# Kernel optimization log

Measured on AMD Instinct MI355X. Metric: run time of the kernel, lower is better.

Reference implementation:

```python
import jax, jax.numpy as jnp
import numpy as np

N, R, T = 40000, 2000, 500000   # node_size, rel_size, triple_size
D, DEPTH, PROXY_N = 128, 2, 64  # node_F, depth, proxy rows
DC = D * (DEPTH + 1)            # 384


def _unique_edges(rng, n_rows, n_cols, n_edges):
    # sorted, duplicate-free edge list -> matches torch.sparse coalesce() ordering
    keys = np.unique(rng.integers(0, n_rows * n_cols, size=int(n_edges * 1.05), dtype=np.int64))[:n_edges]
    assert keys.shape[0] == n_edges
    return np.stack([keys // n_cols, keys % n_cols], axis=1)


def _init_emb(key, r, c):
    w = jax.random.normal(key, (r, c), dtype=jnp.float32)
    return w / jnp.maximum(jnp.linalg.norm(w, axis=1, keepdims=True), 1e-12)


def setup_inputs() -> dict:
    rng = np.random.default_rng(0)
    adj = jnp.asarray(_unique_edges(rng, N, N, T))                    # [T,2] (src, dst)
    idx = jnp.stack([jnp.arange(T), jnp.asarray(rng.integers(0, R, T, dtype=np.int64))], axis=1)  # [T,2]
    val = jnp.ones((T,), jnp.float32)
    ent_m = jnp.asarray(_unique_edges(rng, N, N, T))
    rel_m = jnp.asarray(_unique_edges(rng, N, R, T))
    ks = jax.random.split(jax.random.key(0), 12)
    return {
        "ent_emb": _init_emb(ks[0], N, D),
        "rel_emb": _init_emb(ks[1], R, D),
        "e_gate": _init_emb(ks[2], DC, DC),
        "e_proxy": _init_emb(ks[3], PROXY_N, DC),
        "e_bias": _init_emb(ks[4], 1, DC),
        "e_attn": jnp.stack([_init_emb(ks[5], D, 1), _init_emb(ks[6], D, 1)]),
        "r_gate": _init_emb(ks[7], DC, DC),
        "r_proxy": _init_emb(ks[8], PROXY_N, DC),
        "r_bias": _init_emb(ks[9], 1, DC),
        "r_attn": jnp.stack([_init_emb(ks[10], D, 1), _init_emb(ks[11], D, 1)]),
        "val_input": val,
        "adj_input": adj,
        "index_input": idx,
        "ent_matrix": ent_m,
        "rel_matrix": rel_m,
    }


def _l2(x):
    return x / jnp.maximum(jnp.linalg.norm(x, axis=-1, keepdims=True), 1e-12)


def _seg_softmax(v, seg, n):
    m = jax.ops.segment_max(v, seg, num_segments=n)
    e = jnp.exp(v - m[seg])
    s = jax.ops.segment_sum(e, seg, num_segments=n)
    return e / s[seg]


def _adj_agg(edges, emb, n_rows):
    # torch.sparse.softmax over rows of an all-ones adjacency, then sparse @ emb
    rows, cols = edges[:, 0], edges[:, 1]
    w = _seg_softmax(jnp.zeros(edges.shape[0], emb.dtype), rows, n_rows)
    return jax.ops.segment_sum(w[:, None] * emb[cols], rows, num_segments=n_rows)


def _graph_attention(features, rel_emb, edges, sp_idx, sp_val, attn, gate_k, proxy, bias):
    n = features.shape[0]
    t = sp_val.shape[0]
    feats = jnp.tanh(features)
    outs = [feats]
    for l in range(DEPTH):
        # sparse (T,R) @ rel_emb -> per-edge relation embedding, then L2 normalize
        rels_sum = _l2(jax.ops.segment_sum(sp_val[:, None] * rel_emb[sp_idx[:, 1]], sp_idx[:, 0], num_segments=t))
        neighs = feats[edges[:, 1]]                                   # [T,D]
        neighs = neighs - 2.0 * jnp.sum(neighs * rels_sum, axis=1, keepdims=True) * rels_sum  # Householder reflection
        att = _seg_softmax((rels_sum @ attn[l])[:, 0], edges[:, 0], n)  # sparse row softmax
        feats = jnp.tanh(jax.ops.segment_sum(neighs * att[:, None], edges[:, 0], num_segments=n))
        outs.append(feats)
    outputs = jnp.concatenate(outs, axis=1)                           # [N, DC]
    pa = jax.nn.softmax(_l2(outputs) @ _l2(proxy).T, axis=-1)         # [N, 64]
    pf = outputs - pa @ proxy
    gate = jax.nn.sigmoid(pf @ gate_k + bias)
    return gate * outputs + (1.0 - gate) * pf


def reference(ent_emb, rel_emb, e_gate, e_proxy, e_bias, e_attn, r_gate, r_proxy, r_bias, r_attn, val_input, adj_input, index_input, ent_matrix, rel_matrix):
    ent_feature = _adj_agg(ent_matrix, ent_emb, N)                    # [N,D]
    rel_feature = _adj_agg(rel_matrix, rel_emb, N)                    # [N,D]
    out_e = _graph_attention(ent_feature, rel_emb, adj_input, index_input, val_input, e_attn, e_gate, e_proxy, e_bias)
    out_r = _graph_attention(rel_feature, rel_emb, adj_input, index_input, val_input, r_attn, r_gate, r_proxy, r_bias)
    # dropout_rate = 0.0 -> identity
    return jnp.concatenate([out_e, out_r], axis=-1)                   # [N, 2*DC]
```

## Files before the change

### kernel.cpp

```cpp
#include <hip/hip_runtime.h>
#include <hip/hip_fp16.h>


typedef __attribute__((ext_vector_type(4))) float f32x4;
typedef _Float16 h16x2 __attribute__((ext_vector_type(2)));
typedef _Float16 f16x8 __attribute__((ext_vector_type(8)));
typedef float f32x16 __attribute__((ext_vector_type(16)));

__device__ __forceinline__ float wave_sum(float v) {
#pragma unroll
  for (int o = 32; o > 0; o >>= 1) v += __shfl_xor(v, o, 64);
  return v;
}
__device__ __forceinline__ float wave_max(float v) {
#pragma unroll
  for (int o = 32; o > 0; o >>= 1) v = fmaxf(v, __shfl_xor(v, o, 64));
  return v;
}
__device__ __forceinline__ unsigned pkhalf2(float a, float b) {
  __half2 h = __floats2half2_rn(a, b);
  return __builtin_bit_cast(unsigned, h);
}
__device__ __forceinline__ float bcf(unsigned u) {
  return __builtin_bit_cast(float, u);
}
__device__ __forceinline__ unsigned short f2h(float x) {
  return __builtin_bit_cast(unsigned short, (_Float16)x);
}
__device__ __forceinline__ float h2f(unsigned short h) {
  return (float)__builtin_bit_cast(_Float16, h);
}
__device__ __forceinline__ float tanh_fast(float x) {
  float t = __expf(-2.f * fabsf(x));
  float y = (1.f - t) / (1.f + t);
  return copysignf(y, x);
}
__device__ __forceinline__ float fdot2u(unsigned a, unsigned b, float c) {
#if __has_builtin(__builtin_amdgcn_fdot2)
  return __builtin_amdgcn_fdot2(__builtin_bit_cast(h16x2, a),
                                __builtin_bit_cast(h16x2, b), c, false);
#else
  h16x2 x = __builtin_bit_cast(h16x2, a), y = __builtin_bit_cast(h16x2, b);
  return fmaf((float)x.x, (float)y.x, fmaf((float)x.y, (float)y.y, c));
#endif
}

__global__ void rowptr3_kernel(const int* __restrict__ e0,
                               const int* __restrict__ e1,
                               const int* __restrict__ e2, int T, int N,
                               int* __restrict__ p0, int* __restrict__ p1,
                               int* __restrict__ p2) {
  int tid = blockIdx.x * blockDim.x + threadIdx.x;
  int which = tid / (N + 1);
  int r = tid - which * (N + 1);
  if (which >= 3) return;
  const int* E = which == 0 ? e0 : (which == 1 ? e1 : e2);
  int* P = which == 0 ? p0 : (which == 1 ? p1 : p2);
  int lo = 0, hi = T;
  while (lo < hi) {
    int mid = (lo + hi) >> 1;
    if (E[2 * mid] < r) lo = mid + 1; else hi = mid;
  }
  P[r] = lo;
}

__global__ void relprep_kernel(const float* __restrict__ rel_emb,
                               const float* __restrict__ e_attn,
                               const float* __restrict__ r_attn, int R,
                               float* __restrict__ srel,
                               unsigned* __restrict__ rnorm,
                               unsigned* __restrict__ rel16) {
  int r = blockIdx.x * 4 + (threadIdx.x >> 6);
  int lane = threadIdx.x & 63;
  if (r >= R) return;
  float2 v  = *(const float2*)(rel_emb + (size_t)r * 128 + 2 * lane);
  float2 a0 = *(const float2*)(e_attn + 2 * lane);
  float2 a1 = *(const float2*)(e_attn + 128 + 2 * lane);
  float2 b0 = *(const float2*)(r_attn + 2 * lane);
  float2 b1 = *(const float2*)(r_attn + 128 + 2 * lane);
  float n  = wave_sum(v.x * v.x + v.y * v.y);
  float d0 = wave_sum(v.x * a0.x + v.y * a0.y);
  float d1 = wave_sum(v.x * a1.x + v.y * a1.y);
  float d2 = wave_sum(v.x * b0.x + v.y * b0.y);
  float d3 = wave_sum(v.x * b1.x + v.y * b1.y);
  float inv = 1.f / fmaxf(sqrtf(n), 1e-12f);
  rnorm[(size_t)r * 64 + lane] = pkhalf2(v.x * inv, v.y * inv);
  rel16[(size_t)r * 64 + lane] = pkhalf2(v.x, v.y);
  if (lane == 0) {
    srel[r]          = d0 * inv;
    srel[R + r]      = d1 * inv;
    srel[2 * R + r]  = d2 * inv;
    srel[3 * R + r]  = d3 * inv;
  }
}

__global__ void pack_f16_kernel(const float* __restrict__ src,
                                unsigned* __restrict__ dst, int n2) {
  int i = blockIdx.x * blockDim.x + threadIdx.x;
  if (i >= n2) return;
  float2 v = *(const float2*)(src + 2 * (size_t)i);
  dst[i] = pkhalf2(v.x, v.y);
}

__global__ __launch_bounds__(256) void stats_kernel(
    const int* __restrict__ ptr, const int* __restrict__ idx,
    const float* __restrict__ srel, int R, float* __restrict__ stats, int N) {
  int r = blockIdx.x * 4 + (threadIdx.x >> 6);
  if (r >= N) return;
  int lane = threadIdx.x & 63;
  int beg = ptr[r], end = ptr[r + 1];
  const float* s0 = srel;
  const float* s1 = srel + R;
  const float* s2 = srel + 2 * R;
  const float* s3 = srel + 3 * R;
  float m0 = -INFINITY, m1 = -INFINITY, m2 = -INFINITY, m3 = -INFINITY;
  for (int e = beg + lane; e < end; e += 64) {
    int rel = idx[2 * e + 1];
    m0 = fmaxf(m0, s0[rel]); m1 = fmaxf(m1, s1[rel]);
    m2 = fmaxf(m2, s2[rel]); m3 = fmaxf(m3, s3[rel]);
  }
#pragma unroll
  for (int o = 32; o > 0; o >>= 1) {
    m0 = fmaxf(m0, __shfl_xor(m0, o, 64));
    m1 = fmaxf(m1, __shfl_xor(m1, o, 64));
    m2 = fmaxf(m2, __shfl_xor(m2, o, 64));
    m3 = fmaxf(m3, __shfl_xor(m3, o, 64));
  }
  float d0 = 0.f, d1 = 0.f, d2 = 0.f, d3 = 0.f;
  for (int e = beg + lane; e < end; e += 64) {
    int rel = idx[2 * e + 1];
    d0 += __expf(s0[rel] - m0); d1 += __expf(s1[rel] - m1);
    d2 += __expf(s2[rel] - m2); d3 += __expf(s3[rel] - m3);
  }
#pragma unroll
  for (int o = 32; o > 0; o >>= 1) {
    d0 += __shfl_xor(d0, o, 64); d1 += __shfl_xor(d1, o, 64);
    d2 += __shfl_xor(d2, o, 64); d3 += __shfl_xor(d3, o, 64);
  }
  if (lane == 0) {
    float4 a, b;
    a.x = m0; a.y = (d0 > 0.f) ? 1.f / d0 : 0.f;
    a.z = m1; a.w = (d1 > 0.f) ? 1.f / d1 : 0.f;
    b.x = m2; b.y = (d2 > 0.f) ? 1.f / d2 : 0.f;
    b.z = m3; b.w = (d3 > 0.f) ? 1.f / d3 : 0.f;
    *(float4*)(stats + (size_t)r * 8) = a;
    *(float4*)(stats + (size_t)r * 8 + 4) = b;
  }
}

__global__ void weight_kernel(const int* __restrict__ adj,
                              const int* __restrict__ idx,
                              const float* __restrict__ srel, int R,
                              const float* __restrict__ stats,
                              unsigned* __restrict__ pk,
                              uint2* __restrict__ wt0,
                              uint2* __restrict__ wt1, int T) {
  int e = blockIdx.x * blockDim.x + threadIdx.x;
  if (e >= T) return;
  int row = adj[2 * e];
  int col = adj[2 * e + 1];
  int rel = idx[2 * e + 1];
  float4 a = *(const float4*)(stats + (size_t)row * 8);
  float4 b = *(const float4*)(stats + (size_t)row * 8 + 4);
  float w0 = __expf(srel[rel] - a.x) * a.y;
  float w1 = __expf(srel[R + rel] - a.z) * a.w;
  float w2 = __expf(srel[2 * R + rel] - b.x) * b.y;
  float w3 = __expf(srel[3 * R + rel] - b.z) * b.w;
  pk[e] = (unsigned)col | ((unsigned)rel << 16);
  wt0[e] = make_uint2(__builtin_bit_cast(unsigned, w0),
                      __builtin_bit_cast(unsigned, w2));
  wt1[e] = make_uint2(__builtin_bit_cast(unsigned, w1),
                      __builtin_bit_cast(unsigned, w3));
}

__global__ __launch_bounds__(256) void agg_fused_kernel(
    const int* __restrict__ ptrE, const int* __restrict__ edgesE,
    const unsigned* __restrict__ ent16, const int* __restrict__ ptrR,
    const int* __restrict__ edgesR, const unsigned* __restrict__ rel16,
    unsigned* __restrict__ fout, int N) {
  int r = blockIdx.x * 4 + (threadIdx.x >> 6);
  if (r >= N) return;
  int lane = threadIdx.x & 63;
  int g = lane >> 4, q = lane & 15;

  float aE[8] = {0, 0, 0, 0, 0, 0, 0, 0};
  float aR[8] = {0, 0, 0, 0, 0, 0, 0, 0};

  auto addh = [&](uint4 u, float* a) {
    h16x2 h0 = __builtin_bit_cast(h16x2, u.x), h1 = __builtin_bit_cast(h16x2, u.y);
    h16x2 h2 = __builtin_bit_cast(h16x2, u.z), h3 = __builtin_bit_cast(h16x2, u.w);
    a[0] += (float)h0.x; a[1] += (float)h0.y;
    a[2] += (float)h1.x; a[3] += (float)h1.y;
    a[4] += (float)h2.x; a[5] += (float)h2.y;
    a[6] += (float)h3.x; a[7] += (float)h3.y;
  };

  int begE = ptrE[r], endE = ptrE[r + 1];
  for (int e0 = begE; e0 < endE; e0 += 8) {
    int eA = e0 + g, eB = e0 + 4 + g;
    if (eA < endE)
      addh(*(const uint4*)(ent16 + (size_t)edgesE[2 * eA + 1] * 64 + 4 * q), aE);
    if (eB < endE)
      addh(*(const uint4*)(ent16 + (size_t)edgesE[2 * eB + 1] * 64 + 4 * q), aE);
  }
  int begR = ptrR[r], endR = ptrR[r + 1];
  for (int e0 = begR; e0 < endR; e0 += 8) {
    int eA = e0 + g, eB = e0 + 4 + g;
    if (eA < endR)
      addh(*(const uint4*)(rel16 + (size_t)edgesR[2 * eA + 1] * 64 + 4 * q), aR);
    if (eB < endR)
      addh(*(const uint4*)(rel16 + (size_t)edgesR[2 * eB + 1] * 64 + 4 * q), aR);
  }
#pragma unroll
  for (int j = 0; j < 8; ++j) {
    aE[j] += __shfl_xor(aE[j], 16, 64); aE[j] += __shfl_xor(aE[j], 32, 64);
    aR[j] += __shfl_xor(aR[j], 16, 64); aR[j] += __shfl_xor(aR[j], 32, 64);
  }
  float sE = (endE > begE) ? 1.f / (float)(endE - begE) : 0.f;
  float sR = (endR > begR) ? 1.f / (float)(endR - begR) : 0.f;
  if (g == 0) {
    float t[8];
#pragma unroll
    for (int j = 0; j < 8; ++j) t[j] = tanh_fast(aE[j] * sE);
    uint4 u;
    u.x = pkhalf2(t[0], t[1]); u.y = pkhalf2(t[2], t[3]);
    u.z = pkhalf2(t[4], t[5]); u.w = pkhalf2(t[6], t[7]);
    *(uint4*)(fout + (size_t)r * 128 + 4 * q) = u;
  } else if (g == 1) {
    float t[8];
#pragma unroll
    for (int j = 0; j < 8; ++j) t[j] = tanh_fast(aR[j] * sR);
    uint4 u;
    u.x = pkhalf2(t[0], t[1]); u.y = pkhalf2(t[2], t[3]);
    u.z = pkhalf2(t[4], t[5]); u.w = pkhalf2(t[6], t[7]);
    *(uint4*)(fout + (size_t)r * 128 + 64 + 4 * q) = u;
  }
}

__global__ __launch_bounds__(256) void layer_rec_kernel(
    const int* __restrict__ ptr, const unsigned* __restrict__ pk,
    const uint2* __restrict__ wt, const unsigned* __restrict__ rnorm,
    const unsigned* __restrict__ fin, unsigned* __restrict__ fout,
    int fstride, int N) {
  int r = blockIdx.x * 4 + (threadIdx.x >> 6);
  if (r >= N) return;
  int lane = threadIdx.x & 63;
  int g = lane >> 4, q = lane & 15;
  int beg = ptr[r], end = ptr[r + 1];

  float aE[8] = {0, 0, 0, 0, 0, 0, 0, 0};
  float aR[8] = {0, 0, 0, 0, 0, 0, 0, 0};

  auto accum = [&](uint4 F, uint4 V, float w, float s, float* a) {
    h16x2 f0 = __builtin_bit_cast(h16x2, F.x), v0 = __builtin_bit_cast(h16x2, V.x);
    h16x2 f1 = __builtin_bit_cast(h16x2, F.y), v1 = __builtin_bit_cast(h16x2, V.y);
    h16x2 f2 = __builtin_bit_cast(h16x2, F.z), v2 = __builtin_bit_cast(h16x2, V.z);
    h16x2 f3 = __builtin_bit_cast(h16x2, F.w), v3 = __builtin_bit_cast(h16x2, V.w);
    a[0] = fmaf((float)f0.x, w, fmaf((float)v0.x, s, a[0]));
    a[1] = fmaf((float)f0.y, w, fmaf((float)v0.y, s, a[1]));
    a[2] = fmaf((float)f1.x, w, fmaf((float)v1.x, s, a[2]));
    a[3] = fmaf((float)f1.y, w, fmaf((float)v1.y, s, a[3]));
    a[4] = fmaf((float)f2.x, w, fmaf((float)v2.x, s, a[4]));
    a[5] = fmaf((float)f2.y, w, fmaf((float)v2.y, s, a[5]));
    a[6] = fmaf((float)f3.x, w, fmaf((float)v3.x, s, a[6]));
    a[7] = fmaf((float)f3.y, w, fmaf((float)v3.y, s, a[7]));
  };

  for (int e0 = beg; e0 < end; e0 += 8) {
    int eA = e0 + g, eB = e0 + 4 + g;
    bool actA = eA < end, actB = eB < end;
    unsigned pkA = actA ? pk[eA] : 0u;
    unsigned pkB = actB ? pk[eB] : 0u;
    uint2 wA = actA ? wt[eA] : make_uint2(0u, 0u);
    uint2 wB = actB ? wt[eB] : make_uint2(0u, 0u);
    int colA = (int)(pkA & 0xFFFFu), relA = (int)(pkA >> 16);
    int colB = (int)(pkB & 0xFFFFu), relB = (int)(pkB >> 16);
    float wAE = bcf(wA.x), wAR = bcf(wA.y);
    float wBE = bcf(wB.x), wBR = bcf(wB.y);

    const unsigned* fA = fin + (size_t)colA * 128;
    const unsigned* fB = fin + (size_t)colB * 128;
    uint4 EA = *(const uint4*)(fA + 4 * q);
    uint4 RA = *(const uint4*)(fA + 64 + 4 * q);
    uint4 VA = *(const uint4*)(rnorm + (size_t)relA * 64 + 4 * q);
    uint4 EB = *(const uint4*)(fB + 4 * q);
    uint4 RB = *(const uint4*)(fB + 64 + 4 * q);
    uint4 VB = *(const uint4*)(rnorm + (size_t)relB * 64 + 4 * q);

    float dAE = fdot2u(EA.w, VA.w, fdot2u(EA.z, VA.z,
                fdot2u(EA.y, VA.y, fdot2u(EA.x, VA.x, 0.f))));
    float dAR = fdot2u(RA.w, VA.w, fdot2u(RA.z, VA.z,
                fdot2u(RA.y, VA.y, fdot2u(RA.x, VA.x, 0.f))));
    float dBE = fdot2u(EB.w, VB.w, fdot2u(EB.z, VB.z,
                fdot2u(EB.y, VB.y, fdot2u(EB.x, VB.x, 0.f))));
    float dBR = fdot2u(RB.w, VB.w, fdot2u(RB.z, VB.z,
                fdot2u(RB.y, VB.y, fdot2u(RB.x, VB.x, 0.f))));
#pragma unroll
    for (int m = 1; m < 16; m <<= 1) {
      dAE += __shfl_xor(dAE, m, 64);
      dAR += __shfl_xor(dAR, m, 64);
      dBE += __shfl_xor(dBE, m, 64);
      dBR += __shfl_xor(dBR, m, 64);
    }
    float sAE = -2.f * wAE * dAE, sAR = -2.f * wAR * dAR;
    float sBE = -2.f * wBE * dBE, sBR = -2.f * wBR * dBR;
    accum(EA, VA, wAE, sAE, aE);
    accum(RA, VA, wAR, sAR, aR);
    accum(EB, VB, wBE, sBE, aE);
    accum(RB, VB, wBR, sBR, aR);
  }

#pragma unroll
  for (int j = 0; j < 8; ++j) {
    aE[j] += __shfl_xor(aE[j], 16, 64); aE[j] += __shfl_xor(aE[j], 32, 64);
    aR[j] += __shfl_xor(aR[j], 16, 64); aR[j] += __shfl_xor(aR[j], 32, 64);
  }
  if (g == 0) {
    float t[8];
#pragma unroll
    for (int j = 0; j < 8; ++j) t[j] = tanh_fast(aE[j]);
    uint4 u;
    u.x = pkhalf2(t[0], t[1]); u.y = pkhalf2(t[2], t[3]);
    u.z = pkhalf2(t[4], t[5]); u.w = pkhalf2(t[6], t[7]);
    *(uint4*)(fout + (size_t)r * fstride + 4 * q) = u;
  } else if (g == 1) {
    float t[8];
#pragma unroll
    for (int j = 0; j < 8; ++j) t[j] = tanh_fast(aR[j]);
    uint4 u;
    u.x = pkhalf2(t[0], t[1]); u.y = pkhalf2(t[2], t[3]);
    u.z = pkhalf2(t[4], t[5]); u.w = pkhalf2(t[6], t[7]);
    *(uint4*)(fout + (size_t)r * fstride + 64 + 4 * q) = u;
  }
}

__device__ __forceinline__ void pack_one32(const float* __restrict__ src,
                                           unsigned short* __restrict__ dst,
                                           int NT, int srcld, int mode, int f,
                                           int lane) {
  int kt = f / NT, nt = f % NT;
  int kbase = 16 * kt + 8 * (lane >> 5);
  int n = 32 * nt + (lane & 31);
  unsigned short tmp[8];
#pragma unroll
  for (int j = 0; j < 8; ++j) {
    int k = kbase + j;
    float v = (mode == 0) ? src[(size_t)k * srcld + n] : src[(size_t)n * srcld + k];
    tmp[j] = f2h(v);
  }
  *(uint4*)(dst + ((size_t)f * 64 + lane) * 8) = *(uint4*)tmp;
}
__global__ void pack_all_kernel(const float* eP, const float* eG,
                                const float* rP, const float* rG,
                                unsigned short* b1e, unsigned short* b2e,
                                unsigned short* b3e, unsigned short* b1r,
                                unsigned short* b2r, unsigned short* b3r) {
  int f = blockIdx.x * 4 + (threadIdx.x >> 6);
  int lane = threadIdx.x & 63;
  if (f < 48)       pack_one32(eP, b1e, 2, 384, 1, f, lane);
  else if (f < 96)  pack_one32(eP, b2e, 12, 384, 0, f - 48, lane);
  else if (f < 384) pack_one32(eG, b3e, 12, 384, 0, f - 96, lane);
  else if (f < 432) pack_one32(rP, b1r, 2, 384, 1, f - 384, lane);
  else if (f < 480) pack_one32(rP, b2r, 12, 384, 0, f - 432, lane);
  else if (f < 768) pack_one32(rG, b3r, 12, 384, 0, f - 480, lane);
}

__global__ __launch_bounds__(512) void final_v4_kernel(
    const unsigned* __restrict__ f0, const unsigned* __restrict__ f1,
    const unsigned* __restrict__ f2, int s2, int plane,
    const unsigned short* __restrict__ B1, const unsigned short* __restrict__ B2,
    const unsigned short* __restrict__ B3, const float* __restrict__ bias,
    float* __restrict__ gout, int coloff) {
  __shared__ __align__(16) unsigned sOutH[64][204];
  __shared__ __align__(16) float sPa[64][68];
  __shared__ __align__(16) unsigned short sPaH[64][72];
  __shared__ float sInv[64];
  unsigned short* sOutHs = (unsigned short*)&sOutH[0][0];

  const int t = threadIdx.x;
  const int w = t >> 6, lane = t & 63;
  const int l31 = lane & 31, l5 = lane >> 5;
  const int row0 = blockIdx.x * 64;

  for (int i = t; i < 64 * 48; i += 512) {
    int r = i / 48, c4 = i % 48;
    int buf = c4 >> 4, j = c4 & 15;
    const unsigned* src;
    if (buf == 0)      src = f0 + (size_t)(row0 + r) * 128 + plane + 4 * j;
    else if (buf == 1) src = f1 + (size_t)(row0 + r) * 128 + plane + 4 * j;
    else               src = f2 + (size_t)(row0 + r) * s2 + plane + 4 * j;
    *(uint4*)&sOutH[r][c4 * 4] = *(const uint4*)src;
  }
  __syncthreads();

  for (int rr = 8 * w; rr < 8 * w + 8; ++rr) {
    float s = 0.f;
#pragma unroll
    for (int k = 0; k < 3; ++k) {
      unsigned u = sOutH[rr][3 * lane + k];
      s = fdot2u(u, u, s);
    }
    s = wave_sum(s);
    if (lane == 0) sInv[rr] = 1.f / fmaxf(sqrtf(s), 1e-12f);
  }
  __syncthreads();

  if (w < 4) {
    int rt = w >> 1, ct = w & 1;
    f32x16 acc = {0.f, 0.f, 0.f, 0.f, 0.f, 0.f, 0.f, 0.f,
                  0.f, 0.f, 0.f, 0.f, 0.f, 0.f, 0.f, 0.f};
#pragma unroll
    for (int kt = 0; kt < 24; ++kt) {
      f16x8 a = __builtin_bit_cast(
          f16x8, *(const uint4*)&sOutH[rt * 32 + l31][8 * kt + 4 * l5]);
      f16x8 b = *(const f16x8*)(B1 + ((size_t)(kt * 2 + ct) * 64 + lane) * 8);
      acc = __builtin_amdgcn_mfma_f32_32x32x16_f16(a, b, acc, 0, 0, 0);
    }
#pragma unroll
    for (int reg = 0; reg < 16; ++reg) {
      int row = rt * 32 + (reg & 3) + 8 * (reg >> 2) + 4 * l5;
      sPa[row][ct * 32 + l31] = acc[reg] * sInv[row];
    }
  }
  __syncthreads();

  for (int rr = 8 * w; rr < 8 * w + 8; ++rr) {
    float v = sPa[rr][lane];
    float mx = wave_max(v);
    float e = __expf(v - mx);
    float s = wave_sum(e);
    sPaH[rr][lane] = f2h(e / s);
  }
  __syncthreads();

  const int rt = w & 1, ntb = 3 * (w >> 1);
  unsigned outv[3][8];
  {
    f32x16 acc2[3];
#pragma unroll
    for (int s = 0; s < 3; ++s)
#pragma unroll
      for (int i = 0; i < 16; ++i) acc2[s][i] = 0.f;
#pragma unroll
    for (int kt = 0; kt < 4; ++kt) {
      f16x8 a = __builtin_bit_cast(
          f16x8, *(const uint4*)&sPaH[rt * 32 + l31][16 * kt + 8 * l5]);
#pragma unroll
      for (int s = 0; s < 3; ++s) {
        f16x8 b = *(const f16x8*)(B2 + ((size_t)(kt * 12 + ntb + s) * 64 + lane) * 8);
        acc2[s] = __builtin_amdgcn_mfma_f32_32x32x16_f16(a, b, acc2[s], 0, 0, 0);
      }
    }
#pragma unroll
    for (int s = 0; s < 3; ++s) {
      int col = 32 * (ntb + s) + l31;
#pragma unroll
      for (int p = 0; p < 8; ++p) {
        int ra = rt * 32 + ((2 * p) & 3) + 8 * (p >> 1) + 4 * l5;
        unsigned short u0 = sOutHs[ra * 408 + col];
        unsigned short u1 = sOutHs[(ra + 1) * 408 + col];
        outv[s][p] = (unsigned)u0 | ((unsigned)u1 << 16);
        float pf0 = h2f(u0) - acc2[s][2 * p];
        float pf1 = h2f(u1) - acc2[s][2 * p + 1];
        sOutHs[ra * 408 + col] = f2h(pf0);
        sOutHs[(ra + 1) * 408 + col] = f2h(pf1);
      }
    }
  }
  __syncthreads();

  f32x16 acc3[3];
#pragma unroll
  for (int s = 0; s < 3; ++s)
#pragma unroll
    for (int i = 0; i < 16; ++i) acc3[s][i] = 0.f;
#pragma unroll
  for (int kt = 0; kt < 24; ++kt) {
    f16x8 a = __builtin_bit_cast(
        f16x8, *(const uint4*)&sOutH[rt * 32 + l31][8 * kt + 4 * l5]);
#pragma unroll
    for (int s = 0; s < 3; ++s) {
      f16x8 b = *(const f16x8*)(B3 + ((size_t)(kt * 12 + ntb + s) * 64 + lane) * 8);
      acc3[s] = __builtin_amdgcn_mfma_f32_32x32x16_f16(a, b, acc3[s], 0, 0, 0);
    }
  }

#pragma unroll
  for (int s = 0; s < 3; ++s) {
    int col = 32 * (ntb + s) + l31;
    float bv = bias[col];
#pragma unroll
    for (int p = 0; p < 8; ++p) {
      int ra = rt * 32 + ((2 * p) & 3) + 8 * (p >> 1) + 4 * l5;
      float g0 = 1.f / (1.f + __expf(-(acc3[s][2 * p] + bv)));
      float g1 = 1.f / (1.f + __expf(-(acc3[s][2 * p + 1] + bv)));
      float pf0 = h2f(sOutHs[ra * 408 + col]);
      float pf1 = h2f(sOutHs[(ra + 1) * 408 + col]);
      unsigned ov = outv[s][p];
      float o0 = h2f((unsigned short)(ov & 0xffffu));
      float o1 = h2f((unsigned short)(ov >> 16));
      gout[(size_t)(row0 + ra) * 768 + coloff + col] = g0 * o0 + (1.f - g0) * pf0;
      gout[(size_t)(row0 + ra + 1) * 768 + coloff + col] =
          g1 * o1 + (1.f - g1) * pf1;
    }
  }
}

extern "C" void kernel_launch(void* const* d_in, const int* in_sizes, int n_in,
                              void* d_out, int out_size, void* d_ws,
                              size_t ws_size, hipStream_t stream) {
  (void)n_in; (void)out_size; (void)ws_size;
  const float* ent_emb = (const float*)d_in[0];
  const float* rel_emb = (const float*)d_in[1];
  const float* e_gate  = (const float*)d_in[2];
  const float* e_proxy = (const float*)d_in[3];
  const float* e_bias  = (const float*)d_in[4];
  const float* e_attn  = (const float*)d_in[5];
  const float* r_gate  = (const float*)d_in[6];
  const float* r_proxy = (const float*)d_in[7];
  const float* r_bias  = (const float*)d_in[8];
  const float* r_attn  = (const float*)d_in[9];
  const int* adj   = (const int*)d_in[11];
  const int* idx   = (const int*)d_in[12];
  const int* ent_m = (const int*)d_in[13];
  const int* rel_m = (const int*)d_in[14];
  const int N = in_sizes[0] / 128;
  const int R = in_sizes[1] / 128;
  const int T = in_sizes[10];
  float* out = (float*)d_out;

  char* w = (char*)d_ws;
  size_t used = 0;
  auto alloc = [&](size_t bytes) {
    void* p = (void*)(w + used);
    used += (bytes + 255) & ~(size_t)255;
    return p;
  };
  int* ptr_adj  = (int*)alloc((size_t)(N + 1) * sizeof(int));
  int* ptr_ent  = (int*)alloc((size_t)(N + 1) * sizeof(int));
  int* ptr_rel  = (int*)alloc((size_t)(N + 1) * sizeof(int));
  float* srel   = (float*)alloc((size_t)4 * R * sizeof(float));
  unsigned short* b1e = (unsigned short*)alloc(48 * 1024);
  unsigned short* b2e = (unsigned short*)alloc(48 * 1024);
  unsigned short* b3e = (unsigned short*)alloc(288 * 1024);
  unsigned short* b1r = (unsigned short*)alloc(48 * 1024);
  unsigned short* b2r = (unsigned short*)alloc(48 * 1024);
  unsigned short* b3r = (unsigned short*)alloc(288 * 1024);
  unsigned* rnorm = (unsigned*)alloc((size_t)R * 64 * 4);
  unsigned* rel16 = (unsigned*)alloc((size_t)R * 64 * 4);
  unsigned* ent16 = (unsigned*)alloc((size_t)N * 64 * 4);
  unsigned* fsrc0 = (unsigned*)alloc((size_t)N * 128 * 4);
  unsigned* fsrc1 = (unsigned*)alloc((size_t)N * 128 * 4);
  float* stats = (float*)alloc((size_t)N * 8 * sizeof(float));
  unsigned* pk = (unsigned*)alloc((size_t)T * 4);
  uint2* wt0 = (uint2*)alloc((size_t)T * 8);
  uint2* wt1 = (uint2*)alloc((size_t)T * 8);

  dim3 b256(256);
  rowptr3_kernel<<<(3 * (N + 1) + 255) / 256, b256, 0, stream>>>(
      adj, ent_m, rel_m, T, N, ptr_adj, ptr_ent, ptr_rel);
  relprep_kernel<<<(R + 3) / 4, b256, 0, stream>>>(rel_emb, e_attn, r_attn, R,
                                                   srel, rnorm, rel16);
  pack_f16_kernel<<<(N * 64 + 255) / 256, b256, 0, stream>>>(ent_emb, ent16,
                                                             N * 64);
  pack_all_kernel<<<192, b256, 0, stream>>>(e_proxy, e_gate, r_proxy, r_gate,
                                            b1e, b2e, b3e, b1r, b2r, b3r);

  int grow = (N + 3) / 4;
  stats_kernel<<<grow, b256, 0, stream>>>(ptr_adj, idx, srel, R, stats, N);
  weight_kernel<<<(T + 255) / 256, b256, 0, stream>>>(adj, idx, srel, R, stats,
                                                      pk, wt0, wt1, T);
  agg_fused_kernel<<<grow, b256, 0, stream>>>(ptr_ent, ent_m, ent16, ptr_rel,
                                              rel_m, rel16, fsrc0, N);
  unsigned* gscratch = (unsigned*)out + 512;
  layer_rec_kernel<<<grow, b256, 0, stream>>>(ptr_adj, pk, wt0, rnorm, fsrc0,
                                              fsrc1, 128, N);
  layer_rec_kernel<<<grow, b256, 0, stream>>>(ptr_adj, pk, wt1, rnorm, fsrc1,
                                              gscratch, 768, N);

  int fblocks = (N + 63) / 64;
  final_v4_kernel<<<fblocks, dim3(512), 0, stream>>>(
      fsrc0, fsrc1, gscratch, 768, 0, b1e, b2e, b3e, e_bias, out, 0);
  final_v4_kernel<<<fblocks, dim3(512), 0, stream>>>(
      fsrc0, fsrc1, gscratch, 768, 64, b1r, b2r, b3r, r_bias, out, 384);
}
```

Baseline: 351.6 us.

## Merge entity and relation final kernels into one launch with 32-row blocks

The two final_v4 launches become one final_fused_kernel. Each 256-thread block handles 32 rows for either the entity or the relation side, and the block index picks which. The row L2 norm is now computed while the tile is loaded into shared memory, which removes a separate pass and a barrier. The layer-2 scratch moves to out columns 0 and 704 so each side's writes never overwrite scratch the other side still needs to read. This cuts one kernel launch and the tail between the two launches, and smaller blocks raise occupancy, at the cost of reloading the B matrices per smaller tile.

```diff
diff --git a/kernel.cpp b/kernel.cpp
--- a/kernel.cpp
+++ b/kernel.cpp
@@ -240,8 +240,8 @@
 __global__ __launch_bounds__(256) void layer_rec_kernel(
     const int* __restrict__ ptr, const unsigned* __restrict__ pk,
     const uint2* __restrict__ wt, const unsigned* __restrict__ rnorm,
-    const unsigned* __restrict__ fin, unsigned* __restrict__ fout,
-    int fstride, int N) {
+    const unsigned* __restrict__ fin, unsigned* __restrict__ foutE,
+    unsigned* __restrict__ foutR, int fstride, int N) {
   int r = blockIdx.x * 4 + (threadIdx.x >> 6);
   if (r >= N) return;
   int lane = threadIdx.x & 63;
@@ -322,7 +322,7 @@
     uint4 u;
     u.x = pkhalf2(t[0], t[1]); u.y = pkhalf2(t[2], t[3]);
     u.z = pkhalf2(t[4], t[5]); u.w = pkhalf2(t[6], t[7]);
-    *(uint4*)(fout + (size_t)r * fstride + 4 * q) = u;
+    *(uint4*)(foutE + (size_t)r * fstride + 4 * q) = u;
   } else if (g == 1) {
     float t[8];
 #pragma unroll
@@ -330,7 +330,7 @@
     uint4 u;
     u.x = pkhalf2(t[0], t[1]); u.y = pkhalf2(t[2], t[3]);
     u.z = pkhalf2(t[4], t[5]); u.w = pkhalf2(t[6], t[7]);
-    *(uint4*)(fout + (size_t)r * fstride + 64 + 4 * q) = u;
+    *(uint4*)(foutR + (size_t)r * fstride + 4 * q) = u;
   }
 }
 
@@ -365,60 +365,73 @@
   else if (f < 768) pack_one32(rG, b3r, 12, 384, 0, f - 480, lane);
 }
 
-__global__ __launch_bounds__(512) void final_v4_kernel(
+__global__ __launch_bounds__(256) void final_fused_kernel(
     const unsigned* __restrict__ f0, const unsigned* __restrict__ f1,
-    const unsigned* __restrict__ f2, int s2, int plane,
-    const unsigned short* __restrict__ B1, const unsigned short* __restrict__ B2,
-    const unsigned short* __restrict__ B3, const float* __restrict__ bias,
-    float* __restrict__ gout, int coloff) {
-  __shared__ __align__(16) unsigned sOutH[64][204];
-  __shared__ __align__(16) float sPa[64][68];
-  __shared__ __align__(16) unsigned short sPaH[64][72];
-  __shared__ float sInv[64];
+    const unsigned* __restrict__ outu,
+    const unsigned short* __restrict__ B1e, const unsigned short* __restrict__ B2e,
+    const unsigned short* __restrict__ B3e, const unsigned short* __restrict__ B1r,
+    const unsigned short* __restrict__ B2r, const unsigned short* __restrict__ B3r,
+    const float* __restrict__ biasE, const float* __restrict__ biasR,
+    float* __restrict__ gout) {
+  __shared__ __align__(16) unsigned sOutH[32][204];
+  __shared__ __align__(16) float sPa[32][68];
+  __shared__ __align__(16) unsigned short sPaH[32][72];
+  __shared__ float sInv[32];
   unsigned short* sOutHs = (unsigned short*)&sOutH[0][0];
+
+  const int side = blockIdx.x & 1;
+  const int row0 = (blockIdx.x >> 1) * 32;
+  const int plane = side ? 64 : 0;
+  const unsigned* f2 = outu + (side ? 704 : 0);
+  const unsigned short* B1 = side ? B1r : B1e;
+  const unsigned short* B2 = side ? B2r : B2e;
+  const unsigned short* B3 = side ? B3r : B3e;
+  const float* bias = side ? biasR : biasE;
+  const int coloff = side ? 384 : 0;
 
   const int t = threadIdx.x;
   const int w = t >> 6, lane = t & 63;
   const int l31 = lane & 31, l5 = lane >> 5;
-  const int row0 = blockIdx.x * 64;
-
-  for (int i = t; i < 64 * 48; i += 512) {
-    int r = i / 48, c4 = i % 48;
-    int buf = c4 >> 4, j = c4 & 15;
-    const unsigned* src;
-    if (buf == 0)      src = f0 + (size_t)(row0 + r) * 128 + plane + 4 * j;
-    else if (buf == 1) src = f1 + (size_t)(row0 + r) * 128 + plane + 4 * j;
-    else               src = f2 + (size_t)(row0 + r) * s2 + plane + 4 * j;
-    *(uint4*)&sOutH[r][c4 * 4] = *(const uint4*)src;
+
+  {
+    int rloc = t >> 3;
+    int c0 = t & 7;
+    int rg = row0 + rloc;
+    float ss = 0.f;
+#pragma unroll
+    for (int i = 0; i < 6; ++i) {
+      int c = c0 + 8 * i;
+      int buf = c >> 4, j = c & 15;
+      const unsigned* src;
+      if (buf == 0)      src = f0 + (size_t)rg * 128 + plane + 4 * j;
+      else if (buf == 1) src = f1 + (size_t)rg * 128 + plane + 4 * j;
+      else               src = f2 + (size_t)rg * 768 + 4 * j;
+      uint4 u = *(const uint4*)src;
+      *(uint4*)&sOutH[rloc][c * 4] = u;
+      ss = fdot2u(u.x, u.x, fdot2u(u.y, u.y,
+           fdot2u(u.z, u.z, fdot2u(u.w, u.w, ss))));
+    }
+    ss += __shfl_xor(ss, 1, 64);
+    ss += __shfl_xor(ss, 2, 64);
+    ss += __shfl_xor(ss, 4, 64);
+    if (c0 == 0) sInv[rloc] = 1.f / fmaxf(sqrtf(ss), 1e-12f);
   }
   __syncthreads();
 
-  for (int rr = 8 * w; rr < 8 * w + 8; ++rr) {
-    float s = 0.f;
-#pragma unroll
-    for (int k = 0; k < 3; ++k) {
-      unsigned u = sOutH[rr][3 * lane + k];
-      s = fdot2u(u, u, s);
-    }
-    s = wave_sum(s);
-    if (lane == 0) sInv[rr] = 1.f / fmaxf(sqrtf(s), 1e-12f);
-  }
-  __syncthreads();
-
-  if (w < 4) {
-    int rt = w >> 1, ct = w & 1;
+  if (w < 2) {
+    int ct = w;
     f32x16 acc = {0.f, 0.f, 0.f, 0.f, 0.f, 0.f, 0.f, 0.f,
                   0.f, 0.f, 0.f, 0.f, 0.f, 0.f, 0.f, 0.f};
 #pragma unroll
     for (int kt = 0; kt < 24; ++kt) {
       f16x8 a = __builtin_bit_cast(
-          f16x8, *(const uint4*)&sOutH[rt * 32 + l31][8 * kt + 4 * l5]);
+          f16x8, *(const uint4*)&sOutH[l31][8 * kt + 4 * l5]);
       f16x8 b = *(const f16x8*)(B1 + ((size_t)(kt * 2 + ct) * 64 + lane) * 8);
       acc = __builtin_amdgcn_mfma_f32_32x32x16_f16(a, b, acc, 0, 0, 0);
     }
 #pragma unroll
     for (int reg = 0; reg < 16; ++reg) {
-      int row = rt * 32 + (reg & 3) + 8 * (reg >> 2) + 4 * l5;
+      int row = (reg & 3) + 8 * (reg >> 2) + 4 * l5;
       sPa[row][ct * 32 + l31] = acc[reg] * sInv[row];
     }
   }
@@ -433,7 +446,7 @@
   }
   __syncthreads();
 
-  const int rt = w & 1, ntb = 3 * (w >> 1);
+  const int ntb = 3 * w;
   unsigned outv[3][8];
   {
     f32x16 acc2[3];
@@ -444,7 +457,7 @@
 #pragma unroll
     for (int kt = 0; kt < 4; ++kt) {
       f16x8 a = __builtin_bit_cast(
-          f16x8, *(const uint4*)&sPaH[rt * 32 + l31][16 * kt + 8 * l5]);
+          f16x8, *(const uint4*)&sPaH[l31][16 * kt + 8 * l5]);
 #pragma unroll
       for (int s = 0; s < 3; ++s) {
         f16x8 b = *(const f16x8*)(B2 + ((size_t)(kt * 12 + ntb + s) * 64 + lane) * 8);
@@ -456,7 +469,7 @@
       int col = 32 * (ntb + s) + l31;
 #pragma unroll
       for (int p = 0; p < 8; ++p) {
-        int ra = rt * 32 + ((2 * p) & 3) + 8 * (p >> 1) + 4 * l5;
+        int ra = ((2 * p) & 3) + 8 * (p >> 1) + 4 * l5;
         unsigned short u0 = sOutHs[ra * 408 + col];
         unsigned short u1 = sOutHs[(ra + 1) * 408 + col];
         outv[s][p] = (unsigned)u0 | ((unsigned)u1 << 16);
@@ -477,7 +490,7 @@
 #pragma unroll
   for (int kt = 0; kt < 24; ++kt) {
     f16x8 a = __builtin_bit_cast(
-        f16x8, *(const uint4*)&sOutH[rt * 32 + l31][8 * kt + 4 * l5]);
+        f16x8, *(const uint4*)&sOutH[l31][8 * kt + 4 * l5]);
 #pragma unroll
     for (int s = 0; s < 3; ++s) {
       f16x8 b = *(const f16x8*)(B3 + ((size_t)(kt * 12 + ntb + s) * 64 + lane) * 8);
@@ -491,7 +504,7 @@
     float bv = bias[col];
 #pragma unroll
     for (int p = 0; p < 8; ++p) {
-      int ra = rt * 32 + ((2 * p) & 3) + 8 * (p >> 1) + 4 * l5;
+      int ra = ((2 * p) & 3) + 8 * (p >> 1) + 4 * l5;
       float g0 = 1.f / (1.f + __expf(-(acc3[s][2 * p] + bv)));
       float g1 = 1.f / (1.f + __expf(-(acc3[s][2 * p + 1] + bv)));
       float pf0 = h2f(sOutHs[ra * 408 + col]);
@@ -572,15 +585,13 @@
                                                       pk, wt0, wt1, T);
   agg_fused_kernel<<<grow, b256, 0, stream>>>(ptr_ent, ent_m, ent16, ptr_rel,
                                               rel_m, rel16, fsrc0, N);
-  unsigned* gscratch = (unsigned*)out + 512;
+  unsigned* outu = (unsigned*)out;
   layer_rec_kernel<<<grow, b256, 0, stream>>>(ptr_adj, pk, wt0, rnorm, fsrc0,
-                                              fsrc1, 128, N);
+                                              fsrc1, fsrc1 + 64, 128, N);
   layer_rec_kernel<<<grow, b256, 0, stream>>>(ptr_adj, pk, wt1, rnorm, fsrc1,
-                                              gscratch, 768, N);
-
-  int fblocks = (N + 63) / 64;
-  final_v4_kernel<<<fblocks, dim3(512), 0, stream>>>(
-      fsrc0, fsrc1, gscratch, 768, 0, b1e, b2e, b3e, e_bias, out, 0);
-  final_v4_kernel<<<fblocks, dim3(512), 0, stream>>>(
-      fsrc0, fsrc1, gscratch, 768, 64, b1r, b2r, b3r, r_bias, out, 384);
-}
+                                              outu, outu + 704, 768, N);
+
+  int fblocks = 2 * ((N + 31) / 32);
+  final_fused_kernel<<<fblocks, b256, 0, stream>>>(
+      fsrc0, fsrc1, outu, b1e, b2e, b3e, b1r, b2r, b3r, e_bias, r_bias, out);
+}
```

Result: faster. 293.7 us (-16.5%).
